# Kernel optimization log

Measured on AMD Instinct MI355X. Metric: run time of the kernel, lower is better.

## Reference

```python
import jax, jax.numpy as jnp
import numpy as np

N_NODES = 100000
N_EDGES = 3200000
IN_DIM = 256


def gcn_conv(x, src, dst, W, b):
    # PyG GCNConv: add self-loops, symmetric normalization D^-1/2 A D^-1/2
    n = x.shape[0]
    loop = jnp.arange(n)
    s = jnp.concatenate([src, loop])
    d = jnp.concatenate([dst, loop])
    deg = jax.ops.segment_sum(jnp.ones(d.shape, x.dtype), d, num_segments=n)
    dinv = jnp.where(deg > 0, jax.lax.rsqrt(deg), 0.0).astype(x.dtype)
    norm = dinv[s] * dinv[d]                      # [E+N]
    h = x @ W                                     # [N, out] transform first (out < in)
    msg = h[s] * norm[:, None]                    # gather + scale
    out = jax.ops.segment_sum(msg, d, num_segments=n)  # scatter-add
    return out + b


def setup_inputs() -> dict:
    key = jax.random.key(0)
    ks = jax.random.split(key, 8)
    x = jax.random.normal(ks[0], (N_NODES, IN_DIM), dtype=jnp.float32)
    edge_index = jax.random.randint(ks[1], (2, N_EDGES), 0, N_NODES, dtype=jnp.int64)
    # Glorot-ish scaled params
    W1 = jax.random.normal(ks[2], (IN_DIM, 64), dtype=jnp.float32) / np.sqrt(IN_DIM)
    b1 = jnp.zeros((64,), jnp.float32)
    W2 = jax.random.normal(ks[3], (64, 32), dtype=jnp.float32) / np.sqrt(64)
    b2 = jnp.zeros((32,), jnp.float32)
    fc_w = jax.random.normal(ks[4], (1, 32), dtype=jnp.float32) / np.sqrt(32)
    fc_b = jnp.zeros((1,), jnp.float32)
    return {"x": x, "edge_index": edge_index, "W1": W1, "b1": b1,
            "W2": W2, "b2": b2, "fc_w": fc_w, "fc_b": fc_b}


def reference(x, edge_index, W1, b1, W2, b2, fc_w, fc_b):
    src, dst = edge_index[0], edge_index[1]
    h = jax.nn.relu(gcn_conv(x, src, dst, W1, b1))   # [N, 64]
    h = jax.nn.relu(gcn_conv(h, src, dst, W2, b2))   # [N, 32]
    pooled = h.mean(axis=0)                          # [32]
    return pooled @ fc_w.T + fc_b                    # [1]
```

## Files before the change

### kernel.cpp

```cpp
#include <hip/hip_runtime.h>
#include <hip/hip_fp16.h>

#ifndef F1
#define F1 64
#define F2 32
#endif

#define NBLK 512
#define BSH  7
#define BNODES 128
#define CAP  5120
#define CHMAX 6272

typedef _Float16 half8 __attribute__((ext_vector_type(8)));
typedef float floatx4 __attribute__((ext_vector_type(4)));


__global__ __launch_bounds__(256) void prep0_kernel(float* __restrict__ out,
                                                    int* __restrict__ cnt, int NB) {
    if (threadIdx.x == 0) out[0] = 0.f;
    for (int i = threadIdx.x; i < NB; i += 256) cnt[i] = 0;
}


__global__ __launch_bounds__(256) void scatter_sorted3(const int* __restrict__ src,
                                                       const int* __restrict__ dst,
                                                       int* __restrict__ cnt,
                                                       int* __restrict__ buck,
                                                       const float* __restrict__ W1,
                                                       const float* __restrict__ W2,
                                                       __half* __restrict__ W1t,
                                                       __half* __restrict__ W2t,
                                                       int E, int CH, int NB) {
    int b = blockIdx.x;
    int tid = threadIdx.x;
    if (b == NBLK) {
        for (int e = tid; e < 64 * 256; e += 256) {
            int n = e >> 8, k = e & 255;
            W1t[e] = __float2half(W1[k * 64 + n]);
        }
        for (int e = tid; e < 32 * 64; e += 256) {
            int n = e >> 6, k = e & 63;
            W2t[e] = __float2half(W2[k * 32 + n]);
        }
        return;
    }
    __shared__ int gbase[1024];
    __shared__ int lhist[1024];
    __shared__ int sc[1024];
    __shared__ int lcur[1024];
    __shared__ int sorted[CHMAX];
    __shared__ unsigned short sbkt[CHMAX];
    for (int i = tid; i < 1024; i += 256) lhist[i] = 0;
    __syncthreads();
    int start = b * CH, end = min(E, start + CH);
    int count = end - start;
    for (int e0 = start + tid * 4; e0 < end; e0 += 1024) {
        if (e0 + 4 <= end) {
            int4 d4 = *reinterpret_cast<const int4*>(dst + e0);
            atomicAdd(&lhist[d4.x >> BSH], 1);
            atomicAdd(&lhist[d4.y >> BSH], 1);
            atomicAdd(&lhist[d4.z >> BSH], 1);
            atomicAdd(&lhist[d4.w >> BSH], 1);
        } else {
            for (int e = e0; e < end; ++e) atomicAdd(&lhist[dst[e] >> BSH], 1);
        }
    }
    __syncthreads();
    for (int i = tid; i < 1024; i += 256) {
        int c = lhist[i];
        gbase[i] = (i < NB && c > 0) ? (i * CAP + atomicAdd(&cnt[i], c)) : 0;
        sc[i] = c;
    }
    __syncthreads();
    for (int ofs = 1; ofs < 1024; ofs <<= 1) {
        int i1 = tid + 256, i2 = tid + 512, i3 = tid + 768;
        int v0 = (tid >= ofs) ? sc[tid - ofs] : 0;
        int v1 = (i1 >= ofs) ? sc[i1 - ofs] : 0;
        int v2 = (i2 >= ofs) ? sc[i2 - ofs] : 0;
        int v3 = (i3 >= ofs) ? sc[i3 - ofs] : 0;
        __syncthreads();
        sc[tid] += v0; sc[i1] += v1; sc[i2] += v2; sc[i3] += v3;
        __syncthreads();
    }
    for (int i = tid; i < 1024; i += 256) {
        int ex = sc[i] - lhist[i];
        sc[i] = ex;
        lcur[i] = ex;
    }
    __syncthreads();
    for (int e0 = start + tid * 4; e0 < end; e0 += 1024) {
        if (e0 + 4 <= end) {
            int4 s4 = *reinterpret_cast<const int4*>(src + e0);
            int4 d4 = *reinterpret_cast<const int4*>(dst + e0);
            int k0 = d4.x >> BSH, p0 = atomicAdd(&lcur[k0], 1);
            sorted[p0] = (s4.x << BSH) | (d4.x & (BNODES - 1)); sbkt[p0] = (unsigned short)k0;
            int k1 = d4.y >> BSH, p1 = atomicAdd(&lcur[k1], 1);
            sorted[p1] = (s4.y << BSH) | (d4.y & (BNODES - 1)); sbkt[p1] = (unsigned short)k1;
            int k2 = d4.z >> BSH, p2 = atomicAdd(&lcur[k2], 1);
            sorted[p2] = (s4.z << BSH) | (d4.z & (BNODES - 1)); sbkt[p2] = (unsigned short)k2;
            int k3 = d4.w >> BSH, p3 = atomicAdd(&lcur[k3], 1);
            sorted[p3] = (s4.w << BSH) | (d4.w & (BNODES - 1)); sbkt[p3] = (unsigned short)k3;
        } else {
            for (int e = e0; e < end; ++e) {
                int d = dst[e];
                int k = d >> BSH, p = atomicAdd(&lcur[k], 1);
                sorted[p] = (src[e] << BSH) | (d & (BNODES - 1)); sbkt[p] = (unsigned short)k;
            }
        }
    }
    __syncthreads();
    for (int p = tid; p < count; p += 256) {
        int k = sbkt[p];
        buck[gbase[k] + (p - sc[k])] = sorted[p];
    }
}


__global__ __launch_bounds__(256) void bucket_deg_fill2(const int* __restrict__ buck,
                                                        const int* __restrict__ cnt,
                                                        int* __restrict__ deg,
                                                        float* __restrict__ dinv,
                                                        int* __restrict__ row_off,
                                                        int* __restrict__ csr,
                                                        int N, int NB) {
    __shared__ int bcnt[BNODES];
    __shared__ int sc[BNODES];
    __shared__ int lrow[BNODES];
    __shared__ int lcur[BNODES];
    int k = blockIdx.x;
    int tid = threadIdx.x;
    if (tid < BNODES) { bcnt[tid] = 0; lcur[tid] = 0; }
    __syncthreads();
    int bs = k * CAP;
    int be = bs + cnt[k];
    for (int e = bs + tid; e < be; e += 256)
        atomicAdd(&bcnt[buck[e] & (BNODES - 1)], 1);
    __syncthreads();
    if (tid < BNODES) sc[tid] = bcnt[tid];
    __syncthreads();
    for (int ofs = 1; ofs < BNODES; ofs <<= 1) {
        int v = (tid >= ofs && tid < BNODES) ? sc[tid - ofs] : 0;
        __syncthreads();
        if (tid < BNODES) sc[tid] += v;
        __syncthreads();
    }
    if (tid < BNODES) {
        int excl = sc[tid] - bcnt[tid];
        lrow[tid] = bs + excl;
        int i = (k << BSH) + tid;
        if (i < N) {
            deg[i] = bcnt[tid];
            dinv[i] = rsqrtf((float)(bcnt[tid] + 1));
            row_off[i] = bs + excl;
        }
    }
    __syncthreads();
    for (int e = bs + tid; e < be; e += 256) {
        int p = buck[e];
        int li = p & (BNODES - 1);
        int pos = lrow[li] + atomicAdd(&lcur[li], 1);
        csr[pos] = p >> BSH;
    }
}


__device__ __forceinline__ int swz(int p, int r) { return (p ^ ((r >> 1) & 3)) << 4; }

template <bool AF32, int K, int BN>
__global__ __launch_bounds__(256) void gemm_mfma_kernel(const void* __restrict__ Aptr,
                                                        const __half* __restrict__ Bt,
                                                        const float* __restrict__ dinv,
                                                        __half* __restrict__ C,
                                                        int M) {
    constexpr int NT = BN / 16;
    __shared__ half8 Ash[64 * 4];
    __shared__ half8 Bsh[BN * 4];
    char* Ab = (char*)Ash;
    char* Bb = (char*)Bsh;
    int tid = threadIdx.x;
    int w = tid >> 6;
    int l = tid & 63;
    int row0 = blockIdx.x * 64;
    int sr = tid >> 2, sp = tid & 3;
    int fr = l & 15, fp = l >> 4;
    int arow = w * 16 + fr;
    int a_off = arow * 64 + swz(fp, arow);

    floatx4 acc[NT];
#pragma unroll
    for (int c = 0; c < NT; ++c) acc[c] = (floatx4){0.f, 0.f, 0.f, 0.f};

    for (int k0 = 0; k0 < K; k0 += 32) {
        half8 av = {};
        int gr = row0 + sr;
        if (gr < M) {
            if constexpr (AF32) {
                const float* A = (const float*)Aptr;
                float4 f0 = *(const float4*)(A + (size_t)gr * K + k0 + sp * 8);
                float4 f1 = *(const float4*)(A + (size_t)gr * K + k0 + sp * 8 + 4);
                av[0] = (_Float16)f0.x; av[1] = (_Float16)f0.y;
                av[2] = (_Float16)f0.z; av[3] = (_Float16)f0.w;
                av[4] = (_Float16)f1.x; av[5] = (_Float16)f1.y;
                av[6] = (_Float16)f1.z; av[7] = (_Float16)f1.w;
            } else {
                const __half* A = (const __half*)Aptr;
                av = *(const half8*)(A + (size_t)gr * K + k0 + sp * 8);
            }
        }
        *(half8*)(Ab + sr * 64 + swz(sp, sr)) = av;
        if (tid < BN * 4) {
            int n = tid >> 2, p = tid & 3;
            half8 bv = *(const half8*)(Bt + (size_t)n * K + k0 + p * 8);
            *(half8*)(Bb + n * 64 + swz(p, n)) = bv;
        }
        __syncthreads();
        half8 a = *(const half8*)(Ab + a_off);
#pragma unroll
        for (int c = 0; c < NT; ++c) {
            int col = c * 16 + fr;
            half8 b = *(const half8*)(Bb + col * 64 + swz(fp, col));
            acc[c] = __builtin_amdgcn_mfma_f32_16x16x32_f16(a, b, acc[c], 0, 0, 0);
        }
        __syncthreads();
    }
#pragma unroll
    for (int i = 0; i < 4; ++i) {
        int r = row0 + w * 16 + fp * 4 + i;
        if (r < M) {
            float dn = dinv[r];
#pragma unroll
            for (int c = 0; c < NT; ++c)
                C[(size_t)r * BN + c * 16 + fr] = __float2half(acc[c][i] * dn);
        }
    }
}


__device__ __forceinline__ void acc_row16(const __half* __restrict__ base, float* a) {
    uint4 raw = *reinterpret_cast<const uint4*>(base);
    float2 f0 = __half22float2(*reinterpret_cast<const __half2*>(&raw.x));
    float2 f1 = __half22float2(*reinterpret_cast<const __half2*>(&raw.y));
    float2 f2 = __half22float2(*reinterpret_cast<const __half2*>(&raw.z));
    float2 f3 = __half22float2(*reinterpret_cast<const __half2*>(&raw.w));
    a[0] += f0.x; a[1] += f0.y; a[2] += f1.x; a[3] += f1.y;
    a[4] += f2.x; a[5] += f2.y; a[6] += f3.x; a[7] += f3.y;
}

__device__ __forceinline__ void acc_pk_raw(uint4 raw, __half2* c2) {
    c2[0] = __hadd2(c2[0], *reinterpret_cast<const __half2*>(&raw.x));
    c2[1] = __hadd2(c2[1], *reinterpret_cast<const __half2*>(&raw.y));
    c2[2] = __hadd2(c2[2], *reinterpret_cast<const __half2*>(&raw.z));
    c2[3] = __hadd2(c2[3], *reinterpret_cast<const __half2*>(&raw.w));
}

__device__ __forceinline__ void flush_pk(__half2* c2, float* a) {
#pragma unroll
    for (int j = 0; j < 4; ++j) {
        float2 f = __half22float2(c2[j]);
        a[2 * j] += f.x;
        a[2 * j + 1] += f.y;
        c2[j] = __float2half2_rn(0.f);
    }
}


__global__ __launch_bounds__(256) void agg1_kernel(const __half* __restrict__ g1,
                                                   const int* __restrict__ row_off,
                                                   const int* __restrict__ deg,
                                                   const int* __restrict__ csr,
                                                   const float* __restrict__ dinv,
                                                   const float* __restrict__ b1,
                                                   __half* __restrict__ h1, int n) {
    int node = (blockIdx.x * 256 + threadIdx.x) >> 6;
    int lane = threadIdx.x & 63;
    int g = lane >> 3;
    int f8 = lane & 7;
    if (node >= n) return;
    int start = row_off[node];
    int end = start + deg[node];
    float a[8];
#pragma unroll
    for (int j = 0; j < 8; ++j) a[j] = 0.f;
    if (g == 0)
        acc_row16(g1 + ((size_t)node << 6) + f8 * 8, a);
    __half2 c2[4];
#pragma unroll
    for (int j = 0; j < 4; ++j) c2[j] = __float2half2_rn(0.f);
    int e = start;
    for (; e + 32 <= end; e += 32) {
        int i0 = csr[e + g];
        int i1 = csr[e + 8 + g];
        int i2 = csr[e + 16 + g];
        int i3 = csr[e + 24 + g];
        uint4 r0 = *reinterpret_cast<const uint4*>(g1 + ((size_t)i0 << 6) + f8 * 8);
        uint4 r1 = *reinterpret_cast<const uint4*>(g1 + ((size_t)i1 << 6) + f8 * 8);
        uint4 r2 = *reinterpret_cast<const uint4*>(g1 + ((size_t)i2 << 6) + f8 * 8);
        uint4 r3 = *reinterpret_cast<const uint4*>(g1 + ((size_t)i3 << 6) + f8 * 8);
        acc_pk_raw(r0, c2);
        acc_pk_raw(r1, c2);
        acc_pk_raw(r2, c2);
        acc_pk_raw(r3, c2);
        flush_pk(c2, a);
    }
    if (e + 16 <= end) {
        int i0 = csr[e + g];
        int i1 = csr[e + 8 + g];
        uint4 r0 = *reinterpret_cast<const uint4*>(g1 + ((size_t)i0 << 6) + f8 * 8);
        uint4 r1 = *reinterpret_cast<const uint4*>(g1 + ((size_t)i1 << 6) + f8 * 8);
        acc_pk_raw(r0, c2);
        acc_pk_raw(r1, c2);
        e += 16;
    }
    if (e + 8 <= end) {
        int s = csr[e + g];
        uint4 r = *reinterpret_cast<const uint4*>(g1 + ((size_t)s << 6) + f8 * 8);
        acc_pk_raw(r, c2);
        e += 8;
    }
    if (e + g < end) {
        int s = csr[e + g];
        uint4 r = *reinterpret_cast<const uint4*>(g1 + ((size_t)s << 6) + f8 * 8);
        acc_pk_raw(r, c2);
    }
    flush_pk(c2, a);
#pragma unroll
    for (int j = 0; j < 8; ++j) a[j] += __shfl_xor(a[j], 8);
#pragma unroll
    for (int j = 0; j < 8; ++j) a[j] += __shfl_xor(a[j], 16);
#pragma unroll
    for (int j = 0; j < 8; ++j) a[j] += __shfl_xor(a[j], 32);
    if (g == 0) {
        float dn = dinv[node];
        float4 bl = *reinterpret_cast<const float4*>(b1 + f8 * 8);
        float4 bh = *reinterpret_cast<const float4*>(b1 + f8 * 8 + 4);
        __half hh[8];
        hh[0] = __float2half(fmaxf(a[0] * dn + bl.x, 0.f));
        hh[1] = __float2half(fmaxf(a[1] * dn + bl.y, 0.f));
        hh[2] = __float2half(fmaxf(a[2] * dn + bl.z, 0.f));
        hh[3] = __float2half(fmaxf(a[3] * dn + bl.w, 0.f));
        hh[4] = __float2half(fmaxf(a[4] * dn + bh.x, 0.f));
        hh[5] = __float2half(fmaxf(a[5] * dn + bh.y, 0.f));
        hh[6] = __float2half(fmaxf(a[6] * dn + bh.z, 0.f));
        hh[7] = __float2half(fmaxf(a[7] * dn + bh.w, 0.f));
        *reinterpret_cast<uint4*>(h1 + ((size_t)node << 6) + f8 * 8) =
            *reinterpret_cast<const uint4*>(hh);
    }
}


__global__ __launch_bounds__(256) void agg2_pool_kernel(const __half* __restrict__ g2,
                                                        const int* __restrict__ row_off,
                                                        const int* __restrict__ deg,
                                                        const int* __restrict__ csr,
                                                        const float* __restrict__ dinv,
                                                        const float* __restrict__ b2,
                                                        float* __restrict__ partials,
                                                        int nblocks, int n) {
    int tid = threadIdx.x;
    int half = tid >> 5;
    int node = blockIdx.x * 8 + half;
    int l32 = tid & 31;
    int g = (l32 >> 2);
    int f4 = l32 & 3;
    float a[8];
#pragma unroll
    for (int j = 0; j < 8; ++j) a[j] = 0.f;
    if (node < n) {
        int start = row_off[node];
        int end = start + deg[node];
        if (g == 0)
            acc_row16(g2 + ((size_t)node << 5) + f4 * 8, a);
        __half2 c2[4];
#pragma unroll
        for (int j = 0; j < 4; ++j) c2[j] = __float2half2_rn(0.f);
        int e = start;
        for (; e + 32 <= end; e += 32) {
            int i0 = csr[e + g];
            int i1 = csr[e + 8 + g];
            int i2 = csr[e + 16 + g];
            int i3 = csr[e + 24 + g];
            uint4 r0 = *reinterpret_cast<const uint4*>(g2 + ((size_t)i0 << 5) + f4 * 8);
            uint4 r1 = *reinterpret_cast<const uint4*>(g2 + ((size_t)i1 << 5) + f4 * 8);
            uint4 r2 = *reinterpret_cast<const uint4*>(g2 + ((size_t)i2 << 5) + f4 * 8);
            uint4 r3 = *reinterpret_cast<const uint4*>(g2 + ((size_t)i3 << 5) + f4 * 8);
            acc_pk_raw(r0, c2);
            acc_pk_raw(r1, c2);
            acc_pk_raw(r2, c2);
            acc_pk_raw(r3, c2);
            flush_pk(c2, a);
        }
        if (e + 16 <= end) {
            int i0 = csr[e + g];
            int i1 = csr[e + 8 + g];
            uint4 r0 = *reinterpret_cast<const uint4*>(g2 + ((size_t)i0 << 5) + f4 * 8);
            uint4 r1 = *reinterpret_cast<const uint4*>(g2 + ((size_t)i1 << 5) + f4 * 8);
            acc_pk_raw(r0, c2);
            acc_pk_raw(r1, c2);
            e += 16;
        }
        if (e + 8 <= end) {
            int s = csr[e + g];
            uint4 r = *reinterpret_cast<const uint4*>(g2 + ((size_t)s << 5) + f4 * 8);
            acc_pk_raw(r, c2);
            e += 8;
        }
        if (e + g < end) {
            int s = csr[e + g];
            uint4 r = *reinterpret_cast<const uint4*>(g2 + ((size_t)s << 5) + f4 * 8);
            acc_pk_raw(r, c2);
        }
        flush_pk(c2, a);
#pragma unroll
        for (int j = 0; j < 8; ++j) a[j] += __shfl_xor(a[j], 4);
#pragma unroll
        for (int j = 0; j < 8; ++j) a[j] += __shfl_xor(a[j], 8);
#pragma unroll
        for (int j = 0; j < 8; ++j) a[j] += __shfl_xor(a[j], 16);
    }
    __shared__ float sdata[8][32];
    if (g == 0) {
        float relu[8];
        if (node < n) {
            float dn = dinv[node];
#pragma unroll
            for (int j = 0; j < 8; ++j)
                relu[j] = fmaxf(a[j] * dn + b2[f4 * 8 + j], 0.f);
        } else {
#pragma unroll
            for (int j = 0; j < 8; ++j) relu[j] = 0.f;
        }
#pragma unroll
        for (int j = 0; j < 8; ++j) sdata[half][f4 * 8 + j] = relu[j];
    }
    __syncthreads();
    if (tid < 32) {
        float s = 0.f;
#pragma unroll
        for (int r = 0; r < 8; ++r) s += sdata[r][tid];
        partials[tid * nblocks + blockIdx.x] = s;
    }
}

__global__ __launch_bounds__(256) void reduce_fc_kernel(const float* __restrict__ partials,
                                                        int nblocks,
                                                        const float* __restrict__ fcw,
                                                        const float* __restrict__ fcb,
                                                        float* __restrict__ out, int n) {
    int f = blockIdx.x;
    const float* col = partials + (size_t)f * nblocks;
    float s = 0.f;
    for (int i = threadIdx.x; i < nblocks; i += 256) s += col[i];
    __shared__ float red[256];
    red[threadIdx.x] = s;
    __syncthreads();
    for (int ofs = 128; ofs > 0; ofs >>= 1) {
        if (threadIdx.x < ofs) red[threadIdx.x] += red[threadIdx.x + ofs];
        __syncthreads();
    }
    if (threadIdx.x == 0) {
        float v = (float)((double)red[0] / (double)n * (double)fcw[f]);
        if (f == 0) v += fcb[0];
        atomicAdd(out, v);
    }
}


extern "C" void kernel_launch(void* const* d_in, const int* in_sizes, int n_in,
                              void* d_out, int out_size, void* d_ws, size_t ws_size,
                              hipStream_t stream) {
    const float* x   = (const float*)d_in[0];
    const int*   ei  = (const int*)d_in[1];
    const float* W1  = (const float*)d_in[2];
    const float* b1  = (const float*)d_in[3];
    const float* W2  = (const float*)d_in[4];
    const float* b2  = (const float*)d_in[5];
    const float* fcw = (const float*)d_in[6];
    const float* fcb = (const float*)d_in[7];
    float* out = (float*)d_out;

    const int N = in_sizes[0] / 256;
    const int E = in_sizes[1] / 2;
    const int* src = ei;
    const int* dst = ei + E;

    const int NB = (N + BNODES - 1) >> BSH;
    const int CH = (((E + NBLK - 1) / NBLK) + 3) & ~3;
    const int nb2 = (N + 7) / 8;
    const size_t CAPTOT = (size_t)NB * CAP;

    char* ws = (char*)d_ws;
    size_t off = 0;
    auto alloc = [&](size_t bytes) -> void* {
        void* p = ws + off;
        off = (off + bytes + 255) & ~(size_t)255;
        return p;
    };
    int*   cnt      = (int*)alloc((size_t)NB * 4);
    int*   row_off  = (int*)alloc((size_t)N * 4);
    int*   deg      = (int*)alloc((size_t)N * 4);
    float* dinv     = (float*)alloc((size_t)N * 4);
    int*   csr      = (int*)alloc(CAPTOT * 4);
    __half* W1t     = (__half*)alloc((size_t)64 * 256 * 2);
    __half* W2t     = (__half*)alloc((size_t)32 * 64 * 2);
    size_t szP = CAPTOT * 4;
    size_t szG1 = (size_t)N * F1 * 2;
    void* P = alloc(szP > szG1 ? szP : szG1);
    int*    buck = (int*)P;
    __half* g1   = (__half*)P;
    __half* h1      = (__half*)alloc((size_t)N * F1 * 2);
    __half* g2      = (__half*)alloc((size_t)N * F2 * 2);
    float* partials = (float*)alloc((size_t)F2 * nb2 * 4);

    prep0_kernel<<<1, 256, 0, stream>>>(out, cnt, NB);
    scatter_sorted3<<<NBLK + 1, 256, 0, stream>>>(src, dst, cnt, buck, W1, W2, W1t, W2t, E, CH, NB);
    bucket_deg_fill2<<<NB, 256, 0, stream>>>(buck, cnt, deg, dinv, row_off, csr, N, NB);

    int nbG = (N + 63) / 64;
    gemm_mfma_kernel<true, 256, 64><<<nbG, 256, 0, stream>>>(x, W1t, dinv, g1, N);
    agg1_kernel<<<(N + 3) / 4, 256, 0, stream>>>(g1, row_off, deg, csr, dinv, b1, h1, N);

    gemm_mfma_kernel<false, 64, 32><<<nbG, 256, 0, stream>>>(h1, W2t, dinv, g2, N);
    agg2_pool_kernel<<<nb2, 256, 0, stream>>>(g2, row_off, deg, csr, dinv, b2, partials, nb2, N);

    reduce_fc_kernel<<<F2, 256, 0, stream>>>(partials, nb2, fcw, fcb, out, N);
}
```

Baseline: 194.5 us.

## Fuse layer-2 feature transform GEMM into layer-1 aggregation kernel

```diff
diff --git a/kernel.cpp b/kernel.cpp
--- a/kernel.cpp
+++ b/kernel.cpp
@@ -265,86 +265,118 @@
 }
 
 
-__global__ __launch_bounds__(256) void agg1_kernel(const __half* __restrict__ g1,
-                                                   const int* __restrict__ row_off,
-                                                   const int* __restrict__ deg,
-                                                   const int* __restrict__ csr,
-                                                   const float* __restrict__ dinv,
-                                                   const float* __restrict__ b1,
-                                                   __half* __restrict__ h1, int n) {
-    int node = (blockIdx.x * 256 + threadIdx.x) >> 6;
-    int lane = threadIdx.x & 63;
+__global__ __launch_bounds__(1024) void agg1_fused2(const __half* __restrict__ g1,
+                                                    const int* __restrict__ row_off,
+                                                    const int* __restrict__ deg,
+                                                    const int* __restrict__ csr,
+                                                    const float* __restrict__ dinv,
+                                                    const float* __restrict__ b1,
+                                                    const __half* __restrict__ W2t,
+                                                    __half* __restrict__ g2, int n) {
+    __shared__ __half h1sh[16][72];
+    int tid = threadIdx.x;
+    int wid = tid >> 6;
+    int lane = tid & 63;
+    int node = blockIdx.x * 16 + wid;
     int g = lane >> 3;
     int f8 = lane & 7;
-    if (node >= n) return;
-    int start = row_off[node];
-    int end = start + deg[node];
     float a[8];
 #pragma unroll
     for (int j = 0; j < 8; ++j) a[j] = 0.f;
-    if (g == 0)
-        acc_row16(g1 + ((size_t)node << 6) + f8 * 8, a);
-    __half2 c2[4];
-#pragma unroll
-    for (int j = 0; j < 4; ++j) c2[j] = __float2half2_rn(0.f);
-    int e = start;
-    for (; e + 32 <= end; e += 32) {
-        int i0 = csr[e + g];
-        int i1 = csr[e + 8 + g];
-        int i2 = csr[e + 16 + g];
-        int i3 = csr[e + 24 + g];
-        uint4 r0 = *reinterpret_cast<const uint4*>(g1 + ((size_t)i0 << 6) + f8 * 8);
-        uint4 r1 = *reinterpret_cast<const uint4*>(g1 + ((size_t)i1 << 6) + f8 * 8);
-        uint4 r2 = *reinterpret_cast<const uint4*>(g1 + ((size_t)i2 << 6) + f8 * 8);
-        uint4 r3 = *reinterpret_cast<const uint4*>(g1 + ((size_t)i3 << 6) + f8 * 8);
-        acc_pk_raw(r0, c2);
-        acc_pk_raw(r1, c2);
-        acc_pk_raw(r2, c2);
-        acc_pk_raw(r3, c2);
+    if (node < n) {
+        int start = row_off[node];
+        int end = start + deg[node];
+        if (g == 0)
+            acc_row16(g1 + ((size_t)node << 6) + f8 * 8, a);
+        __half2 c2[4];
+#pragma unroll
+        for (int j = 0; j < 4; ++j) c2[j] = __float2half2_rn(0.f);
+        int e = start;
+        for (; e + 32 <= end; e += 32) {
+            int i0 = csr[e + g];
+            int i1 = csr[e + 8 + g];
+            int i2 = csr[e + 16 + g];
+            int i3 = csr[e + 24 + g];
+            uint4 r0 = *reinterpret_cast<const uint4*>(g1 + ((size_t)i0 << 6) + f8 * 8);
+            uint4 r1 = *reinterpret_cast<const uint4*>(g1 + ((size_t)i1 << 6) + f8 * 8);
+            uint4 r2 = *reinterpret_cast<const uint4*>(g1 + ((size_t)i2 << 6) + f8 * 8);
+            uint4 r3 = *reinterpret_cast<const uint4*>(g1 + ((size_t)i3 << 6) + f8 * 8);
+            acc_pk_raw(r0, c2);
+            acc_pk_raw(r1, c2);
+            acc_pk_raw(r2, c2);
+            acc_pk_raw(r3, c2);
+            flush_pk(c2, a);
+        }
+        if (e + 16 <= end) {
+            int i0 = csr[e + g];
+            int i1 = csr[e + 8 + g];
+            uint4 r0 = *reinterpret_cast<const uint4*>(g1 + ((size_t)i0 << 6) + f8 * 8);
+            uint4 r1 = *reinterpret_cast<const uint4*>(g1 + ((size_t)i1 << 6) + f8 * 8);
+            acc_pk_raw(r0, c2);
+            acc_pk_raw(r1, c2);
+            e += 16;
+        }
+        if (e + 8 <= end) {
+            int s = csr[e + g];
+            uint4 r = *reinterpret_cast<const uint4*>(g1 + ((size_t)s << 6) + f8 * 8);
+            acc_pk_raw(r, c2);
+            e += 8;
+        }
+        if (e + g < end) {
+            int s = csr[e + g];
+            uint4 r = *reinterpret_cast<const uint4*>(g1 + ((size_t)s << 6) + f8 * 8);
+            acc_pk_raw(r, c2);
+        }
         flush_pk(c2, a);
-    }
-    if (e + 16 <= end) {
-        int i0 = csr[e + g];
-        int i1 = csr[e + 8 + g];
-        uint4 r0 = *reinterpret_cast<const uint4*>(g1 + ((size_t)i0 << 6) + f8 * 8);
-        uint4 r1 = *reinterpret_cast<const uint4*>(g1 + ((size_t)i1 << 6) + f8 * 8);
-        acc_pk_raw(r0, c2);
-        acc_pk_raw(r1, c2);
-        e += 16;
-    }
-    if (e + 8 <= end) {
-        int s = csr[e + g];
-        uint4 r = *reinterpret_cast<const uint4*>(g1 + ((size_t)s << 6) + f8 * 8);
-        acc_pk_raw(r, c2);
-        e += 8;
-    }
-    if (e + g < end) {
-        int s = csr[e + g];
-        uint4 r = *reinterpret_cast<const uint4*>(g1 + ((size_t)s << 6) + f8 * 8);
-        acc_pk_raw(r, c2);
-    }
-    flush_pk(c2, a);
-#pragma unroll
-    for (int j = 0; j < 8; ++j) a[j] += __shfl_xor(a[j], 8);
-#pragma unroll
-    for (int j = 0; j < 8; ++j) a[j] += __shfl_xor(a[j], 16);
-#pragma unroll
-    for (int j = 0; j < 8; ++j) a[j] += __shfl_xor(a[j], 32);
+#pragma unroll
+        for (int j = 0; j < 8; ++j) a[j] += __shfl_xor(a[j], 8);
+#pragma unroll
+        for (int j = 0; j < 8; ++j) a[j] += __shfl_xor(a[j], 16);
+#pragma unroll
+        for (int j = 0; j < 8; ++j) a[j] += __shfl_xor(a[j], 32);
+    }
     if (g == 0) {
-        float dn = dinv[node];
-        float4 bl = *reinterpret_cast<const float4*>(b1 + f8 * 8);
-        float4 bh = *reinterpret_cast<const float4*>(b1 + f8 * 8 + 4);
         __half hh[8];
-        hh[0] = __float2half(fmaxf(a[0] * dn + bl.x, 0.f));
-        hh[1] = __float2half(fmaxf(a[1] * dn + bl.y, 0.f));
-        hh[2] = __float2half(fmaxf(a[2] * dn + bl.z, 0.f));
-        hh[3] = __float2half(fmaxf(a[3] * dn + bl.w, 0.f));
-        hh[4] = __float2half(fmaxf(a[4] * dn + bh.x, 0.f));
-        hh[5] = __float2half(fmaxf(a[5] * dn + bh.y, 0.f));
-        hh[6] = __float2half(fmaxf(a[6] * dn + bh.z, 0.f));
-        hh[7] = __float2half(fmaxf(a[7] * dn + bh.w, 0.f));
-        *reinterpret_cast<uint4*>(h1 + ((size_t)node << 6) + f8 * 8) =
-            *reinterpret_cast<const uint4*>(hh);
+        if (node < n) {
+            float dn = dinv[node];
+            float4 bl = *reinterpret_cast<const float4*>(b1 + f8 * 8);
+            float4 bh = *reinterpret_cast<const float4*>(b1 + f8 * 8 + 4);
+            hh[0] = __float2half(fmaxf(a[0] * dn + bl.x, 0.f));
+            hh[1] = __float2half(fmaxf(a[1] * dn + bl.y, 0.f));
+            hh[2] = __float2half(fmaxf(a[2] * dn + bl.z, 0.f));
+            hh[3] = __float2half(fmaxf(a[3] * dn + bl.w, 0.f));
+            hh[4] = __float2half(fmaxf(a[4] * dn + bh.x, 0.f));
+            hh[5] = __float2half(fmaxf(a[5] * dn + bh.y, 0.f));
+            hh[6] = __float2half(fmaxf(a[6] * dn + bh.z, 0.f));
+            hh[7] = __float2half(fmaxf(a[7] * dn + bh.w, 0.f));
+        } else {
+#pragma unroll
+            for (int j = 0; j < 8; ++j) hh[j] = __float2half(0.f);
+        }
+        *reinterpret_cast<uint4*>(&h1sh[wid][f8 * 8]) = *reinterpret_cast<const uint4*>(hh);
+    }
+    __syncthreads();
+    if (tid < 64) {
+        int fr = tid & 15, fp = tid >> 4;
+        floatx4 acc0 = (floatx4){0.f, 0.f, 0.f, 0.f};
+        floatx4 acc1 = (floatx4){0.f, 0.f, 0.f, 0.f};
+#pragma unroll
+        for (int k0 = 0; k0 < 64; k0 += 32) {
+            half8 av = *reinterpret_cast<const half8*>(&h1sh[fr][k0 + fp * 8]);
+            half8 b0 = *reinterpret_cast<const half8*>(W2t + (size_t)fr * 64 + k0 + fp * 8);
+            half8 b1v = *reinterpret_cast<const half8*>(W2t + (size_t)(16 + fr) * 64 + k0 + fp * 8);
+            acc0 = __builtin_amdgcn_mfma_f32_16x16x32_f16(av, b0, acc0, 0, 0, 0);
+            acc1 = __builtin_amdgcn_mfma_f32_16x16x32_f16(av, b1v, acc1, 0, 0, 0);
+        }
+#pragma unroll
+        for (int i = 0; i < 4; ++i) {
+            int r = blockIdx.x * 16 + fp * 4 + i;
+            if (r < n) {
+                float dn = dinv[r];
+                g2[(size_t)r * 32 + fr] = __float2half(acc0[i] * dn);
+                g2[(size_t)r * 32 + 16 + fr] = __float2half(acc1[i] * dn);
+            }
+        }
     }
 }
 
@@ -508,7 +540,6 @@
     void* P = alloc(szP > szG1 ? szP : szG1);
     int*    buck = (int*)P;
     __half* g1   = (__half*)P;
-    __half* h1      = (__half*)alloc((size_t)N * F1 * 2);
     __half* g2      = (__half*)alloc((size_t)N * F2 * 2);
     float* partials = (float*)alloc((size_t)F2 * nb2 * 4);
 
@@ -518,9 +549,8 @@
 
     int nbG = (N + 63) / 64;
     gemm_mfma_kernel<true, 256, 64><<<nbG, 256, 0, stream>>>(x, W1t, dinv, g1, N);
-    agg1_kernel<<<(N + 3) / 4, 256, 0, stream>>>(g1, row_off, deg, csr, dinv, b1, h1, N);
-
-    gemm_mfma_kernel<false, 64, 32><<<nbG, 256, 0, stream>>>(h1, W2t, dinv, g2, N);
+    agg1_fused2<<<(N + 15) / 16, 1024, 0, stream>>>(g1, row_off, deg, csr, dinv, b1, W2t, g2, N);
+
     agg2_pool_kernel<<<nb2, 256, 0, stream>>>(g2, row_off, deg, csr, dinv, b2, partials, nb2, N);
 
     reduce_fc_kernel<<<F2, 256, 0, stream>>>(partials, nb2, fcw, fcb, out, N);
```

Result: slower. 208.9 us (+7.4%).
